# Kernel tuning notes

Hardware: AMD Instinct MI355X
Metric: run time of the kernel (lower is better)

The kernel has to match this reference:

```python
import jax, jax.numpy as jnp
import numpy as np

N = 50000          # nodes
E = 1600000        # edges (avg degree 32)
F_IN = 1280        # ESM node feature dim
H = 128            # hidden (128x0e irreps)
G = 64             # graphs in batch
OUT = 2
SH0 = 0.5 / np.sqrt(np.pi)   # Y_00 under e3nn 'integral' normalization (constant; l=1,2 sh
                             # have zero CG coupling into 0e outputs, so only l=0 survives)
TP_NORM = SH0 / np.sqrt(H)   # path weight normalization 1/sqrt(fan_in), fan_in = mul_in1*mul_in2 = H*1


def _mean_aggregate(msg, dst, num_nodes):
    # scatter-mean of per-edge messages onto destination nodes (PyG aggr='mean')
    s = jax.ops.segment_sum(msg, dst, num_segments=num_nodes)
    cnt = jax.ops.segment_sum(jnp.ones((msg.shape[0],), msg.dtype), dst, num_segments=num_nodes)
    return s / jnp.maximum(cnt, 1.0)[:, None]


def _equivariant_conv(h, edge_index, tp_w):
    # EquivariantConv: gather x_j, tensor product with sh(edge_vec), scatter-mean.
    # edge_vec normalization is irrelevant for the surviving l=0 path (Y_00 is constant).
    src, dst = edge_index[0], edge_index[1]
    msg = (h[src] @ tp_w) * TP_NORM            # [E, H]
    return _mean_aggregate(msg, dst, h.shape[0])


def setup_inputs() -> dict:
    key = jax.random.key(0)
    ks = jax.random.split(key, 16)
    inp = {
        "x": jax.random.normal(ks[0], (N, F_IN), jnp.float32),
        "pos": jax.random.normal(ks[1], (N, 3), jnp.float32),
        "edge_index": jax.random.randint(ks[2], (2, E), 0, N),
        "batch": jnp.sort(jax.random.randint(ks[3], (N,), 0, G)),
        # lin_in (xavier-like scale)
        "lin_w": jax.random.normal(ks[4], (F_IN, H), jnp.float32) * (1.0 / np.sqrt(F_IN)),
        "lin_b": jnp.zeros((H,), jnp.float32),
        # FullyConnectedTensorProduct internal weights ~ N(0,1), shape [mul_in, mul_out]
        "tp_w1": jax.random.normal(ks[5], (H, H), jnp.float32),
        "tp_w2": jax.random.normal(ks[6], (H, H), jnp.float32),
        "tp_w3": jax.random.normal(ks[7], (H, H), jnp.float32),
        # classifier
        "c1w": jax.random.normal(ks[8], (H, H), jnp.float32) * (1.0 / np.sqrt(H)),
        "c1b": jnp.zeros((H,), jnp.float32),
        "c2w": jax.random.normal(ks[9], (H, H), jnp.float32) * (1.0 / np.sqrt(H)),
        "c2b": jnp.zeros((H,), jnp.float32),
        "c3w": jax.random.normal(ks[10], (H, OUT), jnp.float32) * (1.0 / np.sqrt(H)),
        "c3b": jnp.zeros((OUT,), jnp.float32),
    }
    return inp


def reference(x, pos, edge_index, batch, lin_w, lin_b, tp_w1, tp_w2, tp_w3,
              c1w, c1b, c2w, c2b, c3w, c3b):
    h = jax.nn.relu(x @ lin_w + lin_b)                    # lin_in + relu (dropout p=0, eval)
    h = jax.nn.relu(_equivariant_conv(h, edge_index, tp_w1))
    h = jax.nn.relu(_equivariant_conv(h, edge_index, tp_w2))
    h = _equivariant_conv(h, edge_index, tp_w3)           # no relu after conv3
    # global_mean_pool over graphs
    s = jax.ops.segment_sum(h, batch, num_segments=G)
    cnt = jax.ops.segment_sum(jnp.ones((h.shape[0],), h.dtype), batch, num_segments=G)
    z = s / jnp.maximum(cnt, 1.0)[:, None]                # [G, H]
    o = jax.nn.relu(z @ c1w + c1b)
    o = jax.nn.relu(o @ c2w + c2b)
    out = o @ c3w + c3b                                   # [G, OUT]
    return (out, z)
```

## Files before the change

kernel.cpp:

```cpp
#include <hip/hip_runtime.h>
#include <hip/hip_bf16.h>

typedef __bf16 bf16_t;
typedef bf16_t bf16x4 __attribute__((ext_vector_type(4)));
typedef bf16_t bf16x8 __attribute__((ext_vector_type(8)));
typedef float f32x4 __attribute__((ext_vector_type(4)));

static constexpr int N_NODES = 50000;
static constexpr int N_EDGES = 1600000;
static constexpr int FIN = 1280;
static constexpr int HD = 128;
static constexpr int NG = 64;
static constexpr float TP_NORM_F = 0.0249338908f;

__global__ __launch_bounds__(256) void k_transpose_scale(const float* __restrict__ src,
                                                         bf16_t* __restrict__ dst,
                                                         int K, float scale) {
  int idx = blockIdx.x * 256 + threadIdx.x;
  if (idx >= K * HD) return;
  int k = idx >> 7, n = idx & 127;
  dst[n * K + k] = (bf16_t)(src[idx] * scale);
}

template <typename AT>
__global__ __launch_bounds__(256) void k_gemm64(const AT* __restrict__ A,
                                                const bf16_t* __restrict__ Bt,
                                                const float* __restrict__ bias,
                                                bf16_t* __restrict__ C,
                                                int M, int K, int doRelu) {
  __shared__ bf16_t As[64 * 64];
  __shared__ bf16_t Bs[128 * 64];
  const int t = threadIdx.x;
  const int wid = t >> 6;
  const int lane = t & 63;
  const int wm = (wid & 1) * 32;
  const int wn = (wid >> 1) * 64;
  const int l15 = lane & 15;
  const int quad = lane >> 4;
  const int rowBase = blockIdx.x * 64;

  f32x4 acc[2][4];
#pragma unroll
  for (int i = 0; i < 2; ++i)
#pragma unroll
    for (int j = 0; j < 4; ++j) {
      f32x4 z = {0.f, 0.f, 0.f, 0.f};
      acc[i][j] = z;
    }

  for (int k0 = 0; k0 < K; k0 += 64) {
    if constexpr (sizeof(AT) == 4) {
#pragma unroll
      for (int i = 0; i < 4; ++i) {
        int idx = t + i * 256;
        int row = idx >> 4;
        int col4 = idx & 15;
        int gr = rowBase + row;
        float4 v = make_float4(0.f, 0.f, 0.f, 0.f);
        if (gr < M) v = *(const float4*)(A + (size_t)gr * K + k0 + col4 * 4);
        bf16x4 w;
        w[0] = (bf16_t)v.x; w[1] = (bf16_t)v.y; w[2] = (bf16_t)v.z; w[3] = (bf16_t)v.w;
        int c = col4 >> 1;
        int off = row * 64 + ((c ^ (row & 7)) << 3) + ((col4 & 1) << 2);
        *(bf16x4*)&As[off] = w;
      }
    } else {
#pragma unroll
      for (int i = 0; i < 2; ++i) {
        int idx = t + i * 256;
        int row = idx >> 3;
        int c = idx & 7;
        int gr = rowBase + row;
        bf16x8 v = {};
        if (gr < M) v = *(const bf16x8*)(A + (size_t)gr * K + k0 + c * 8);
        int off = row * 64 + ((c ^ (row & 7)) << 3);
        *(bf16x8*)&As[off] = v;
      }
    }
#pragma unroll
    for (int i = 0; i < 4; ++i) {
      int idx = t + i * 256;
      int row = idx >> 3;
      int c = idx & 7;
      bf16x8 v = *(const bf16x8*)(Bt + (size_t)row * K + k0 + c * 8);
      int off = row * 64 + ((c ^ (row & 7)) << 3);
      *(bf16x8*)&Bs[off] = v;
    }
    __syncthreads();
#pragma unroll
    for (int kk = 0; kk < 2; ++kk) {
      bf16x8 af[2], bfr[4];
      int k8 = kk * 4 + quad;
#pragma unroll
      for (int mi = 0; mi < 2; ++mi) {
        int row = wm + mi * 16 + l15;
        af[mi] = *(const bf16x8*)&As[row * 64 + ((k8 ^ (row & 7)) << 3)];
      }
#pragma unroll
      for (int ni = 0; ni < 4; ++ni) {
        int row = wn + ni * 16 + l15;
        bfr[ni] = *(const bf16x8*)&Bs[row * 64 + ((k8 ^ (row & 7)) << 3)];
      }
#pragma unroll
      for (int mi = 0; mi < 2; ++mi)
#pragma unroll
        for (int ni = 0; ni < 4; ++ni)
          acc[mi][ni] = __builtin_amdgcn_mfma_f32_16x16x32_bf16(af[mi], bfr[ni], acc[mi][ni], 0, 0, 0);
    }
    __syncthreads();
  }

#pragma unroll
  for (int mi = 0; mi < 2; ++mi) {
#pragma unroll
    for (int ni = 0; ni < 4; ++ni) {
      int col = wn + ni * 16 + l15;
      float bv = bias ? bias[col] : 0.f;
#pragma unroll
      for (int r = 0; r < 4; ++r) {
        int row = wm + mi * 16 + quad * 4 + r;
        int gr = rowBase + row;
        if (gr < M) {
          float v = acc[mi][ni][r] + bv;
          if (doRelu) v = fmaxf(v, 0.f);
          C[(size_t)gr * HD + col] = (bf16_t)v;
        }
      }
    }
  }
}

__global__ __launch_bounds__(256) void k_pos(const int* __restrict__ dst, int* __restrict__ cnt,
                                             int* __restrict__ pos, int E) {
  int e = blockIdx.x * 256 + threadIdx.x;
  if (e < E) pos[e] = atomicAdd(&cnt[dst[e]], 1);
}

__global__ __launch_bounds__(1024) void k_scan(const int* __restrict__ cnt, int* __restrict__ off, int n) {
  __shared__ int s[1024];
  int t = threadIdx.x;
  const int CH = (n + 1023) / 1024;
  int base = t * CH;
  int sum = 0;
  for (int i = 0; i < CH; ++i) {
    int j = base + i;
    if (j < n) sum += cnt[j];
  }
  s[t] = sum;
  __syncthreads();
  for (int d = 1; d < 1024; d <<= 1) {
    int x = (t >= d) ? s[t - d] : 0;
    __syncthreads();
    s[t] += x;
    __syncthreads();
  }
  int excl = s[t] - sum;
  for (int i = 0; i < CH; ++i) {
    int j = base + i;
    if (j < n) {
      off[j] = excl;
      excl += cnt[j];
    }
  }
  if (t == 1023) off[n] = s[1023];
}

__global__ __launch_bounds__(256) void k_fill(const int* __restrict__ src, const int* __restrict__ dst,
                                              const int* __restrict__ off, const int* __restrict__ pos,
                                              int* __restrict__ ssrc, int E) {
  int e = blockIdx.x * 256 + threadIdx.x;
  if (e >= E) return;
  ssrc[off[dst[e]] + pos[e]] = src[e];
}

__global__ __launch_bounds__(256) void k_aggregate(const bf16_t* __restrict__ h,
                                                   const int* __restrict__ ssrc,
                                                   const int* __restrict__ off,
                                                   bf16_t* __restrict__ agg, int n) {
  int node = blockIdx.x * 16 + (threadIdx.x >> 4);
  int lane = threadIdx.x & 15;
  if (node >= n) return;
  int b = off[node], e = off[node + 1];
  float acc[8];
#pragma unroll
  for (int j = 0; j < 8; ++j) acc[j] = 0.f;
  const bf16_t* hp = h + lane * 8;
  int i = b;
  for (; i + 4 <= e; i += 4) {
    int s0 = ssrc[i], s1 = ssrc[i + 1], s2 = ssrc[i + 2], s3 = ssrc[i + 3];
    bf16x8 v0 = *(const bf16x8*)(hp + (size_t)s0 * HD);
    bf16x8 v1 = *(const bf16x8*)(hp + (size_t)s1 * HD);
    bf16x8 v2 = *(const bf16x8*)(hp + (size_t)s2 * HD);
    bf16x8 v3 = *(const bf16x8*)(hp + (size_t)s3 * HD);
#pragma unroll
    for (int j = 0; j < 8; ++j)
      acc[j] += ((float)v0[j] + (float)v1[j]) + ((float)v2[j] + (float)v3[j]);
  }
  for (; i < e; ++i) {
    int s0 = ssrc[i];
    bf16x8 v0 = *(const bf16x8*)(hp + (size_t)s0 * HD);
#pragma unroll
    for (int j = 0; j < 8; ++j) acc[j] += (float)v0[j];
  }
  float inv = (e > b) ? 1.f / (float)(e - b) : 0.f;
  bf16x8 o;
#pragma unroll
  for (int j = 0; j < 8; ++j) o[j] = (bf16_t)(acc[j] * inv);
  *(bf16x8*)(agg + (size_t)node * HD + lane * 8) = o;
}

__global__ __launch_bounds__(128) void k_pool(const bf16_t* __restrict__ agg, const int* __restrict__ batch,
                                              float* __restrict__ p, float* __restrict__ gcnt, int n) {
  int base = blockIdx.x * 256;
  if (base >= n) return;
  int t = threadIdx.x;
  int end = min(base + 256, n);
  float acc = 0.f;
  int curg = batch[base];
  int runStart = base;
  for (int i = base; i < end; ++i) {
    int g = batch[i];
    if (g != curg) {
      atomicAdd(&p[curg * HD + t], acc);
      if (t == 0) atomicAdd(&gcnt[curg], (float)(i - runStart));
      acc = 0.f; curg = g; runStart = i;
    }
    acc += (float)agg[(size_t)i * HD + t];
  }
  atomicAdd(&p[curg * HD + t], acc);
  if (t == 0) atomicAdd(&gcnt[curg], (float)(end - runStart));
}

__global__ __launch_bounds__(128) void k_head(const float* __restrict__ p, const float* __restrict__ gcnt,
                                              const float* __restrict__ w3,
                                              const float* __restrict__ c1w, const float* __restrict__ c1b,
                                              const float* __restrict__ c2w, const float* __restrict__ c2b,
                                              const float* __restrict__ c3w, const float* __restrict__ c3b,
                                              float* __restrict__ out) {
  __shared__ float sa[128], sb[128];
  int g = blockIdx.x, t = threadIdx.x;
  float inv = 1.f / fmaxf(gcnt[g], 1.f);
  sa[t] = p[g * HD + t] * inv;
  __syncthreads();
  float z = 0.f;
  for (int k = 0; k < HD; ++k) z += sa[k] * w3[k * HD + t];
  z *= TP_NORM_F;
  out[128 + g * HD + t] = z;
  sb[t] = z;
  __syncthreads();
  float o1 = c1b[t];
  for (int k = 0; k < HD; ++k) o1 += sb[k] * c1w[k * HD + t];
  o1 = fmaxf(o1, 0.f);
  __syncthreads();
  sa[t] = o1;
  __syncthreads();
  float o2 = c2b[t];
  for (int k = 0; k < HD; ++k) o2 += sa[k] * c2w[k * HD + t];
  o2 = fmaxf(o2, 0.f);
  __syncthreads();
  sb[t] = o2;
  __syncthreads();
  if (t < 2) {
    float o = c3b[t];
    for (int k = 0; k < HD; ++k) o += sb[k] * c3w[k * 2 + t];
    out[g * 2 + t] = o;
  }
}

extern "C" void kernel_launch(void* const* d_in, const int* in_sizes, int n_in,
                              void* d_out, int out_size, void* d_ws, size_t ws_size,
                              hipStream_t stream) {
  const float* x = (const float*)d_in[0];
  const int* eidx = (const int*)d_in[2];
  const int* src = eidx;
  const int* dst = eidx + N_EDGES;
  const int* batch = (const int*)d_in[3];
  const float* lin_w = (const float*)d_in[4];
  const float* lin_b = (const float*)d_in[5];
  const float* tp_w1 = (const float*)d_in[6];
  const float* tp_w2 = (const float*)d_in[7];
  const float* tp_w3 = (const float*)d_in[8];
  const float* c1w = (const float*)d_in[9];
  const float* c1b = (const float*)d_in[10];
  const float* c2w = (const float*)d_in[11];
  const float* c2b = (const float*)d_in[12];
  const float* c3w = (const float*)d_in[13];
  const float* c3b = (const float*)d_in[14];
  float* out = (float*)d_out;
  (void)in_sizes; (void)n_in; (void)out_size; (void)ws_size;

  uintptr_t wp = (uintptr_t)d_ws;
  auto alloc = [&](size_t bytes) -> void* {
    uintptr_t a = (wp + 255) & ~(uintptr_t)255;
    wp = a + bytes;
    return (void*)a;
  };
  bf16_t* WtL  = (bf16_t*)alloc(sizeof(bf16_t) * (size_t)HD * FIN);
  bf16_t* Wt1  = (bf16_t*)alloc(sizeof(bf16_t) * (size_t)HD * HD);
  bf16_t* Wt2  = (bf16_t*)alloc(sizeof(bf16_t) * (size_t)HD * HD);
  bf16_t* h    = (bf16_t*)alloc(sizeof(bf16_t) * (size_t)50048 * HD);
  bf16_t* agg  = (bf16_t*)alloc(sizeof(bf16_t) * (size_t)50048 * HD);
  int*    cnt  = (int*)alloc(sizeof(int) * N_NODES);
  int*    offs = (int*)alloc(sizeof(int) * (N_NODES + 1));
  int*    pos  = (int*)alloc(sizeof(int) * N_EDGES);
  int*    ssrc = (int*)alloc(sizeof(int) * N_EDGES);
  float*  pbuf = (float*)alloc(sizeof(float) * NG * HD);
  float*  gcnt = (float*)alloc(sizeof(float) * NG);

  hipMemsetAsync(cnt, 0, sizeof(int) * N_NODES, stream);
  hipMemsetAsync(pbuf, 0, sizeof(float) * NG * HD, stream);
  hipMemsetAsync(gcnt, 0, sizeof(float) * NG, stream);

  k_transpose_scale<<<(FIN * HD + 255) / 256, 256, 0, stream>>>(lin_w, WtL, FIN, 1.0f);
  k_transpose_scale<<<(HD * HD + 255) / 256, 256, 0, stream>>>(tp_w1, Wt1, HD, TP_NORM_F);
  k_transpose_scale<<<(HD * HD + 255) / 256, 256, 0, stream>>>(tp_w2, Wt2, HD, TP_NORM_F);

  k_pos<<<(N_EDGES + 255) / 256, 256, 0, stream>>>(dst, cnt, pos, N_EDGES);
  k_scan<<<1, 1024, 0, stream>>>(cnt, offs, N_NODES);
  k_fill<<<(N_EDGES + 255) / 256, 256, 0, stream>>>(src, dst, offs, pos, ssrc, N_EDGES);

  const int gblocks = (N_NODES + 63) / 64;
  const int ablocks = (N_NODES + 15) / 16;

  k_gemm64<float><<<gblocks, 256, 0, stream>>>(x, WtL, lin_b, h, N_NODES, FIN, 1);

  k_aggregate<<<ablocks, 256, 0, stream>>>(h, ssrc, offs, agg, N_NODES);
  k_gemm64<bf16_t><<<gblocks, 256, 0, stream>>>(agg, Wt1, nullptr, h, N_NODES, HD, 1);
  k_aggregate<<<ablocks, 256, 0, stream>>>(h, ssrc, offs, agg, N_NODES);
  k_gemm64<bf16_t><<<gblocks, 256, 0, stream>>>(agg, Wt2, nullptr, h, N_NODES, HD, 1);
  k_aggregate<<<ablocks, 256, 0, stream>>>(h, ssrc, offs, agg, N_NODES);

  k_pool<<<(N_NODES + 255) / 256, 128, 0, stream>>>(agg, batch, pbuf, gcnt, N_NODES);
  k_head<<<NG, 128, 0, stream>>>(pbuf, gcnt, tp_w3, c1w, c1b, c2w, c2b, c3w, c3b, out);
}
```

Baseline: 878.2 us.

## Parallelize scan, widen aggregation per node, shrink GEMM row tile

Replaces the single-block prefix scan with a three-kernel block-reduce/scan/add scheme so the CSR offset computation uses many CUs. Assigns a full 64-lane wavefront per node in aggregation, with four lane groups splitting edges and reducing partial sums through shuffles, to raise memory parallelism on the gathers. Halves the GEMM row tile to 32 so more blocks run, at the cost of less reuse of the weight tile. Adds two extra kernel launches and shuffle reductions.

```diff
diff --git a/kernel.cpp b/kernel.cpp
--- a/kernel.cpp
+++ b/kernel.cpp
@@ -23,27 +23,26 @@
 }
 
 template <typename AT>
-__global__ __launch_bounds__(256) void k_gemm64(const AT* __restrict__ A,
+__global__ __launch_bounds__(256) void k_gemm32(const AT* __restrict__ A,
                                                 const bf16_t* __restrict__ Bt,
                                                 const float* __restrict__ bias,
                                                 bf16_t* __restrict__ C,
                                                 int M, int K, int doRelu) {
-  __shared__ bf16_t As[64 * 64];
+  __shared__ bf16_t As[32 * 64];
   __shared__ bf16_t Bs[128 * 64];
   const int t = threadIdx.x;
   const int wid = t >> 6;
   const int lane = t & 63;
-  const int wm = (wid & 1) * 32;
-  const int wn = (wid >> 1) * 64;
+  const int wn = wid * 32;
   const int l15 = lane & 15;
   const int quad = lane >> 4;
-  const int rowBase = blockIdx.x * 64;
-
-  f32x4 acc[2][4];
+  const int rowBase = blockIdx.x * 32;
+
+  f32x4 acc[2][2];
 #pragma unroll
   for (int i = 0; i < 2; ++i)
 #pragma unroll
-    for (int j = 0; j < 4; ++j) {
+    for (int j = 0; j < 2; ++j) {
       f32x4 z = {0.f, 0.f, 0.f, 0.f};
       acc[i][j] = z;
     }
@@ -51,7 +50,7 @@
   for (int k0 = 0; k0 < K; k0 += 64) {
     if constexpr (sizeof(AT) == 4) {
 #pragma unroll
-      for (int i = 0; i < 4; ++i) {
+      for (int i = 0; i < 2; ++i) {
         int idx = t + i * 256;
         int row = idx >> 4;
         int col4 = idx & 15;
@@ -65,17 +64,13 @@
         *(bf16x4*)&As[off] = w;
       }
     } else {
-#pragma unroll
-      for (int i = 0; i < 2; ++i) {
-        int idx = t + i * 256;
-        int row = idx >> 3;
-        int c = idx & 7;
-        int gr = rowBase + row;
-        bf16x8 v = {};
-        if (gr < M) v = *(const bf16x8*)(A + (size_t)gr * K + k0 + c * 8);
-        int off = row * 64 + ((c ^ (row & 7)) << 3);
-        *(bf16x8*)&As[off] = v;
-      }
+      int row = t >> 3;
+      int c = t & 7;
+      int gr = rowBase + row;
+      bf16x8 v = {};
+      if (gr < M) v = *(const bf16x8*)(A + (size_t)gr * K + k0 + c * 8);
+      int off = row * 64 + ((c ^ (row & 7)) << 3);
+      *(bf16x8*)&As[off] = v;
     }
 #pragma unroll
     for (int i = 0; i < 4; ++i) {
@@ -89,22 +84,22 @@
     __syncthreads();
 #pragma unroll
     for (int kk = 0; kk < 2; ++kk) {
-      bf16x8 af[2], bfr[4];
+      bf16x8 af[2], bfr[2];
       int k8 = kk * 4 + quad;
 #pragma unroll
       for (int mi = 0; mi < 2; ++mi) {
-        int row = wm + mi * 16 + l15;
+        int row = mi * 16 + l15;
         af[mi] = *(const bf16x8*)&As[row * 64 + ((k8 ^ (row & 7)) << 3)];
       }
 #pragma unroll
-      for (int ni = 0; ni < 4; ++ni) {
+      for (int ni = 0; ni < 2; ++ni) {
         int row = wn + ni * 16 + l15;
         bfr[ni] = *(const bf16x8*)&Bs[row * 64 + ((k8 ^ (row & 7)) << 3)];
       }
 #pragma unroll
       for (int mi = 0; mi < 2; ++mi)
 #pragma unroll
-        for (int ni = 0; ni < 4; ++ni)
+        for (int ni = 0; ni < 2; ++ni)
           acc[mi][ni] = __builtin_amdgcn_mfma_f32_16x16x32_bf16(af[mi], bfr[ni], acc[mi][ni], 0, 0, 0);
     }
     __syncthreads();
@@ -113,12 +108,12 @@
 #pragma unroll
   for (int mi = 0; mi < 2; ++mi) {
 #pragma unroll
-    for (int ni = 0; ni < 4; ++ni) {
+    for (int ni = 0; ni < 2; ++ni) {
       int col = wn + ni * 16 + l15;
       float bv = bias ? bias[col] : 0.f;
 #pragma unroll
       for (int r = 0; r < 4; ++r) {
-        int row = wm + mi * 16 + quad * 4 + r;
+        int row = mi * 16 + quad * 4 + r;
         int gr = rowBase + row;
         if (gr < M) {
           float v = acc[mi][ni][r] + bv;
@@ -136,33 +131,51 @@
   if (e < E) pos[e] = atomicAdd(&cnt[dst[e]], 1);
 }
 
-__global__ __launch_bounds__(1024) void k_scan(const int* __restrict__ cnt, int* __restrict__ off, int n) {
-  __shared__ int s[1024];
+__global__ __launch_bounds__(256) void k_scan1(const int* __restrict__ cnt, int* __restrict__ bsum, int n) {
+  __shared__ int s[256];
   int t = threadIdx.x;
-  const int CH = (n + 1023) / 1024;
-  int base = t * CH;
-  int sum = 0;
-  for (int i = 0; i < CH; ++i) {
-    int j = base + i;
-    if (j < n) sum += cnt[j];
-  }
-  s[t] = sum;
-  __syncthreads();
-  for (int d = 1; d < 1024; d <<= 1) {
+  int i = blockIdx.x * 256 + t;
+  s[t] = (i < n) ? cnt[i] : 0;
+  __syncthreads();
+  for (int d = 128; d > 0; d >>= 1) {
+    if (t < d) s[t] += s[t + d];
+    __syncthreads();
+  }
+  if (t == 0) bsum[blockIdx.x] = s[0];
+}
+
+__global__ __launch_bounds__(256) void k_scan2(int* __restrict__ bsum, int nb) {
+  __shared__ int s[256];
+  int t = threadIdx.x;
+  int v = (t < nb) ? bsum[t] : 0;
+  s[t] = v;
+  __syncthreads();
+  for (int d = 1; d < 256; d <<= 1) {
     int x = (t >= d) ? s[t - d] : 0;
     __syncthreads();
     s[t] += x;
     __syncthreads();
   }
-  int excl = s[t] - sum;
-  for (int i = 0; i < CH; ++i) {
-    int j = base + i;
-    if (j < n) {
-      off[j] = excl;
-      excl += cnt[j];
-    }
-  }
-  if (t == 1023) off[n] = s[1023];
+  if (t < nb) bsum[t] = s[t] - v;
+  if (t == 255) bsum[nb] = s[255];
+}
+
+__global__ __launch_bounds__(256) void k_scan3(const int* __restrict__ cnt, const int* __restrict__ bsum,
+                                               int* __restrict__ off, int n) {
+  __shared__ int s[256];
+  int t = threadIdx.x;
+  int i = blockIdx.x * 256 + t;
+  int v = (i < n) ? cnt[i] : 0;
+  s[t] = v;
+  __syncthreads();
+  for (int d = 1; d < 256; d <<= 1) {
+    int x = (t >= d) ? s[t - d] : 0;
+    __syncthreads();
+    s[t] += x;
+    __syncthreads();
+  }
+  if (i < n) off[i] = bsum[blockIdx.x] + s[t] - v;
+  if (i == n - 1) off[n] = bsum[blockIdx.x] + s[t];
 }
 
 __global__ __launch_bounds__(256) void k_fill(const int* __restrict__ src, const int* __restrict__ dst,
@@ -177,36 +190,50 @@
                                                    const int* __restrict__ ssrc,
                                                    const int* __restrict__ off,
                                                    bf16_t* __restrict__ agg, int n) {
-  int node = blockIdx.x * 16 + (threadIdx.x >> 4);
-  int lane = threadIdx.x & 15;
+  int node = blockIdx.x * 4 + (threadIdx.x >> 6);
   if (node >= n) return;
+  int lane = threadIdx.x & 63;
+  int g = lane >> 4;
+  int fl = lane & 15;
   int b = off[node], e = off[node + 1];
   float acc[8];
 #pragma unroll
   for (int j = 0; j < 8; ++j) acc[j] = 0.f;
-  const bf16_t* hp = h + lane * 8;
+  const bf16_t* hp = h + fl * 8;
   int i = b;
-  for (; i + 4 <= e; i += 4) {
-    int s0 = ssrc[i], s1 = ssrc[i + 1], s2 = ssrc[i + 2], s3 = ssrc[i + 3];
+  for (; i + 8 <= e; i += 8) {
+    int s0 = ssrc[i + g];
+    int s1 = ssrc[i + 4 + g];
     bf16x8 v0 = *(const bf16x8*)(hp + (size_t)s0 * HD);
     bf16x8 v1 = *(const bf16x8*)(hp + (size_t)s1 * HD);
-    bf16x8 v2 = *(const bf16x8*)(hp + (size_t)s2 * HD);
-    bf16x8 v3 = *(const bf16x8*)(hp + (size_t)s3 * HD);
-#pragma unroll
-    for (int j = 0; j < 8; ++j)
-      acc[j] += ((float)v0[j] + (float)v1[j]) + ((float)v2[j] + (float)v3[j]);
-  }
-  for (; i < e; ++i) {
-    int s0 = ssrc[i];
+#pragma unroll
+    for (int j = 0; j < 8; ++j) acc[j] += (float)v0[j] + (float)v1[j];
+  }
+  if (i + 4 <= e) {
+    int s0 = ssrc[i + g];
     bf16x8 v0 = *(const bf16x8*)(hp + (size_t)s0 * HD);
 #pragma unroll
     for (int j = 0; j < 8; ++j) acc[j] += (float)v0[j];
-  }
-  float inv = (e > b) ? 1.f / (float)(e - b) : 0.f;
-  bf16x8 o;
-#pragma unroll
-  for (int j = 0; j < 8; ++j) o[j] = (bf16_t)(acc[j] * inv);
-  *(bf16x8*)(agg + (size_t)node * HD + lane * 8) = o;
+    i += 4;
+  }
+  if (i + g < e) {
+    int s0 = ssrc[i + g];
+    bf16x8 v0 = *(const bf16x8*)(hp + (size_t)s0 * HD);
+#pragma unroll
+    for (int j = 0; j < 8; ++j) acc[j] += (float)v0[j];
+  }
+#pragma unroll
+  for (int j = 0; j < 8; ++j) {
+    acc[j] += __shfl_xor(acc[j], 16);
+    acc[j] += __shfl_xor(acc[j], 32);
+  }
+  if (g == 0) {
+    float inv = (e > b) ? 1.f / (float)(e - b) : 0.f;
+    bf16x8 o;
+#pragma unroll
+    for (int j = 0; j < 8; ++j) o[j] = (bf16_t)(acc[j] * inv);
+    *(bf16x8*)(agg + (size_t)node * HD + fl * 8) = o;
+  }
 }
 
 __global__ __launch_bounds__(128) void k_pool(const bf16_t* __restrict__ agg, const int* __restrict__ batch,
@@ -301,6 +328,7 @@
   bf16_t* h    = (bf16_t*)alloc(sizeof(bf16_t) * (size_t)50048 * HD);
   bf16_t* agg  = (bf16_t*)alloc(sizeof(bf16_t) * (size_t)50048 * HD);
   int*    cnt  = (int*)alloc(sizeof(int) * N_NODES);
+  int*    bsum = (int*)alloc(sizeof(int) * 256);
   int*    offs = (int*)alloc(sizeof(int) * (N_NODES + 1));
   int*    pos  = (int*)alloc(sizeof(int) * N_EDGES);
   int*    ssrc = (int*)alloc(sizeof(int) * N_EDGES);
@@ -315,19 +343,22 @@
   k_transpose_scale<<<(HD * HD + 255) / 256, 256, 0, stream>>>(tp_w1, Wt1, HD, TP_NORM_F);
   k_transpose_scale<<<(HD * HD + 255) / 256, 256, 0, stream>>>(tp_w2, Wt2, HD, TP_NORM_F);
 
+  const int nScanBlocks = (N_NODES + 255) / 256;
   k_pos<<<(N_EDGES + 255) / 256, 256, 0, stream>>>(dst, cnt, pos, N_EDGES);
-  k_scan<<<1, 1024, 0, stream>>>(cnt, offs, N_NODES);
+  k_scan1<<<nScanBlocks, 256, 0, stream>>>(cnt, bsum, N_NODES);
+  k_scan2<<<1, 256, 0, stream>>>(bsum, nScanBlocks);
+  k_scan3<<<nScanBlocks, 256, 0, stream>>>(cnt, bsum, offs, N_NODES);
   k_fill<<<(N_EDGES + 255) / 256, 256, 0, stream>>>(src, dst, offs, pos, ssrc, N_EDGES);
 
-  const int gblocks = (N_NODES + 63) / 64;
-  const int ablocks = (N_NODES + 15) / 16;
-
-  k_gemm64<float><<<gblocks, 256, 0, stream>>>(x, WtL, lin_b, h, N_NODES, FIN, 1);
+  const int gblocks = (N_NODES + 31) / 32;
+  const int ablocks = (N_NODES + 3) / 4;
+
+  k_gemm32<float><<<gblocks, 256, 0, stream>>>(x, WtL, lin_b, h, N_NODES, FIN, 1);
 
   k_aggregate<<<ablocks, 256, 0, stream>>>(h, ssrc, offs, agg, N_NODES);
-  k_gemm64<bf16_t><<<gblocks, 256, 0, stream>>>(agg, Wt1, nullptr, h, N_NODES, HD, 1);
+  k_gemm32<bf16_t><<<gblocks, 256, 0, stream>>>(agg, Wt1, nullptr, h, N_NODES, HD, 1);
   k_aggregate<<<ablocks, 256, 0, stream>>>(h, ssrc, offs, agg, N_NODES);
-  k_gemm64<bf16_t><<<gblocks, 256, 0, stream>>>(agg, Wt2, nullptr, h, N_NODES, HD, 1);
+  k_gemm32<bf16_t><<<gblocks, 256, 0, stream>>>(agg, Wt2, nullptr, h, N_NODES, HD, 1);
   k_aggregate<<<ablocks, 256, 0, stream>>>(h, ssrc, offs, agg, N_NODES);
 
   k_pool<<<(N_NODES + 255) / 256, 128, 0, stream>>>(agg, batch, pbuf, gcnt, N_NODES);
```

Result: faster. 782.2 us (-10.9%).
